# Kernel optimization log

Measured on AMD Instinct MI355X. Metric: run time of the kernel, lower is better.

## Reference

```python
import jax, jax.numpy as jnp
import numpy as np

HEADS = 16
D_MODEL = 1024
GROUP = 4
SEQ = 2048
HEAD_DIM = D_MODEL // HEADS          # 64
KV_HEADS = HEADS // GROUP            # 4


def rope_tables(head_dim, seq_len, base=10000.0):
    # NOTE: faithful to source: exp = -2*arange(0,d,2)/d  (steps of 2 -> base^{-4j/d})
    exp = -2.0 * jnp.arange(0, head_dim, 2, dtype=jnp.float32) / head_dim
    thetas = jnp.power(base, exp)                       # [d/2]
    m = jnp.arange(seq_len, dtype=jnp.float32)          # [S]
    freq = jnp.outer(m, thetas)                         # [S, d/2]
    return jnp.cos(freq), jnp.sin(freq)


def apply_rope(x, cos, sin):
    # x: [B,S,H,D]; complex rotation on consecutive pairs
    B, S, H, D = x.shape
    xr = x.reshape(B, S, H, D // 2, 2)
    x0, x1 = xr[..., 0], xr[..., 1]
    c = cos[None, :S, None, :]
    s = sin[None, :S, None, :]
    out = jnp.stack([x0 * c - x1 * s, x0 * s + x1 * c], axis=-1)
    return out.reshape(B, S, H, D)


def setup_inputs() -> dict:
    key = jax.random.key(0)
    ks = jax.random.split(key, 8)
    B = 1
    q = jax.random.normal(ks[0], (B, SEQ, D_MODEL), dtype=jnp.float32)
    k = jax.random.normal(ks[1], (B, SEQ, D_MODEL), dtype=jnp.float32)
    v = jax.random.normal(ks[2], (B, SEQ, D_MODEL), dtype=jnp.float32)
    mask = jnp.tril(jnp.ones((SEQ, SEQ), dtype=jnp.int32))[None]  # causal [B,S,S]
    sc = 0.02
    Wq = jax.random.normal(ks[3], (D_MODEL, D_MODEL), dtype=jnp.float32) * sc
    Wk = jax.random.normal(ks[4], (D_MODEL, D_MODEL // GROUP), dtype=jnp.float32) * sc
    Wv = jax.random.normal(ks[5], (D_MODEL, D_MODEL // GROUP), dtype=jnp.float32) * sc
    Wo = jax.random.normal(ks[6], (D_MODEL, D_MODEL), dtype=jnp.float32) * sc
    bq = jnp.zeros((D_MODEL,), jnp.float32)
    bk = jnp.zeros((D_MODEL // GROUP,), jnp.float32)
    bv = jnp.zeros((D_MODEL // GROUP,), jnp.float32)
    bo = jnp.zeros((D_MODEL,), jnp.float32)
    return {"q": q, "k": k, "v": v, "mask": mask, "Wq": Wq, "bq": bq,
            "Wk": Wk, "bk": bk, "Wv": Wv, "bv": bv, "Wo": Wo, "bo": bo}


def reference(q, k, v, mask, Wq, bq, Wk, bk, Wv, bv, Wo, bo):
    B, S, _ = q.shape
    cos, sin = rope_tables(HEAD_DIM, S)
    qh = (q @ Wq + bq).reshape(B, S, HEADS, HEAD_DIM)
    kh = (k @ Wk + bk).reshape(B, S, KV_HEADS, HEAD_DIM)
    vh = (v @ Wv + bv).reshape(B, S, KV_HEADS, HEAD_DIM)
    qh = apply_rope(qh, cos, sin)
    kh = apply_rope(kh, cos, sin)
    qh = qh.transpose(0, 2, 1, 3)                       # [B,H,S,D]
    kh = kh.transpose(0, 2, 1, 3)                       # [B,Hkv,S,D]
    vh = vh.transpose(0, 2, 1, 3)
    # torch .repeat tiles: query head j attends kv head j % KV_HEADS
    kh = jnp.tile(kh, (1, GROUP, 1, 1))                 # [B,H,S,D]
    vh = jnp.tile(vh, (1, GROUP, 1, 1))
    scores = jnp.einsum('bhqd,bhkd->bhqk', qh, kh) / jnp.sqrt(
        jnp.asarray(HEAD_DIM, dtype=qh.dtype))
    scores = jnp.where(mask[:, None, :, :] == 0, -jnp.inf, scores)
    attn = jax.nn.softmax(scores, axis=-1)
    out = jnp.einsum('bhqk,bhkd->bhqd', attn, vh)
    out = out.transpose(0, 2, 1, 3).reshape(B, S, D_MODEL)
    return out @ Wo + bo
```

## Files before the change

kernel.cpp:

```cpp
#include <hip/hip_runtime.h>
#include <hip/hip_bf16.h>
#include <math.h>


#define SEQ 2048
#define DM 1024
#define HD 64

using u16 = unsigned short;
typedef __attribute__((ext_vector_type(8))) short bf16x8;
typedef __attribute__((ext_vector_type(4))) float f32x4;

#define QSCALE 0.18033688011112042f

__device__ __forceinline__ u16 f2b(float f) {
    union { float f; unsigned int i; } v; v.f = f;
    unsigned int u = v.i;
    return (u16)((u + 0x7fffu + ((u >> 16) & 1u)) >> 16);
}
__device__ __forceinline__ short f2b_fast(float f) {
    union { float f; unsigned int i; } v; v.f = f;
    return (short)((v.i + 0x8000u) >> 16);
}

__global__ __launch_bounds__(256) void prep_kernel(
    const float* __restrict__ Wq, const float* __restrict__ Wk,
    const float* __restrict__ Wv, const float* __restrict__ Wo,
    u16* __restrict__ Wt, u16* __restrict__ wot)
{
    __shared__ short T[64][72];
    const int tid = blockIdx.x;
    const float* W; u16* dstB; int N, t0, rowoff;
    if (tid < 256)      { W = Wq; dstB = Wt;  N = 1024; t0 = tid;       rowoff = 0; }
    else if (tid < 320) { W = Wk; dstB = Wt;  N = 256;  t0 = tid - 256; rowoff = 1024; }
    else if (tid < 384) { W = Wv; dstB = Wt;  N = 256;  t0 = tid - 320; rowoff = 1280; }
    else                { W = Wo; dstB = wot; N = 1024; t0 = tid - 384; rowoff = 0; }
    const int ntn = N >> 6;
    const int k0 = (t0 / ntn) * 64, n0 = (t0 % ntn) * 64;
    const int t = threadIdx.x;
    {
        const int r = t >> 4, c4 = (t & 15) * 4;
        #pragma unroll
        for (int rr = 0; rr < 4; ++rr) {
            const int k = r + rr * 16;
            float4 wv4 = *reinterpret_cast<const float4*>(W + (size_t)(k0 + k) * N + n0 + c4);
            T[c4 + 0][k] = (short)f2b(wv4.x);
            T[c4 + 1][k] = (short)f2b(wv4.y);
            T[c4 + 2][k] = (short)f2b(wv4.z);
            T[c4 + 3][k] = (short)f2b(wv4.w);
        }
    }
    __syncthreads();
    {
        const int n = t >> 2, ck = (t & 3) * 16;
        u16* dst = dstB + (size_t)(rowoff + n0 + n) * DM + k0 + ck;
        *reinterpret_cast<bf16x8*>(dst)     = *reinterpret_cast<const bf16x8*>(&T[n][ck]);
        *reinterpret_cast<bf16x8*>(dst + 8) = *reinterpret_cast<const bf16x8*>(&T[n][ck + 8]);
    }
}

__global__ __launch_bounds__(256) void proj_mfma(
    const float* __restrict__ qin, const float* __restrict__ kin, const float* __restrict__ vin,
    const u16* __restrict__ Wt,
    const float* __restrict__ bq, const float* __restrict__ bk, const float* __restrict__ bv,
    u16* __restrict__ Qr, u16* __restrict__ Kr, u16* __restrict__ Vrt)
{
    const int n0 = blockIdx.x * 64, m0 = blockIdx.y * 64;
    const int zone = (n0 < 1024) ? 0 : (n0 < 1280) ? 1 : 2;
    const float* __restrict__ src = (zone == 0) ? qin : (zone == 1) ? kin : vin;

    __shared__ short As[64][72];
    __shared__ short Bs[64][72];

    const int t = threadIdx.x;
    const int w = t >> 6, lane = t & 63, lm = lane & 15, quad = lane >> 4;
    const int sr = t >> 2, sc = (t & 3) * 16;

    f32x4 acc[4] = { {0,0,0,0}, {0,0,0,0}, {0,0,0,0}, {0,0,0,0} };

    for (int k0 = 0; k0 < DM; k0 += 64) {
        const float* ap = src + (size_t)(m0 + sr) * DM + k0 + sc;
        float4 a0 = *reinterpret_cast<const float4*>(ap);
        float4 a1 = *reinterpret_cast<const float4*>(ap + 4);
        float4 a2 = *reinterpret_cast<const float4*>(ap + 8);
        float4 a3 = *reinterpret_cast<const float4*>(ap + 12);
        bf16x8 v0, v1;
        v0[0] = (short)f2b(a0.x); v0[1] = (short)f2b(a0.y);
        v0[2] = (short)f2b(a0.z); v0[3] = (short)f2b(a0.w);
        v0[4] = (short)f2b(a1.x); v0[5] = (short)f2b(a1.y);
        v0[6] = (short)f2b(a1.z); v0[7] = (short)f2b(a1.w);
        v1[0] = (short)f2b(a2.x); v1[1] = (short)f2b(a2.y);
        v1[2] = (short)f2b(a2.z); v1[3] = (short)f2b(a2.w);
        v1[4] = (short)f2b(a3.x); v1[5] = (short)f2b(a3.y);
        v1[6] = (short)f2b(a3.z); v1[7] = (short)f2b(a3.w);
        *reinterpret_cast<bf16x8*>(&As[sr][sc])     = v0;
        *reinterpret_cast<bf16x8*>(&As[sr][sc + 8]) = v1;
        const u16* bp = Wt + (size_t)(n0 + sr) * DM + k0 + sc;
        *reinterpret_cast<bf16x8*>(&Bs[sr][sc])     = *reinterpret_cast<const bf16x8*>(bp);
        *reinterpret_cast<bf16x8*>(&Bs[sr][sc + 8]) = *reinterpret_cast<const bf16x8*>(bp + 8);
        __syncthreads();
        bf16x8 af0 = *reinterpret_cast<const bf16x8*>(&As[16 * w + lm][quad * 8]);
        bf16x8 af1 = *reinterpret_cast<const bf16x8*>(&As[16 * w + lm][32 + quad * 8]);
        #pragma unroll
        for (int nb = 0; nb < 4; ++nb) {
            bf16x8 b0 = *reinterpret_cast<const bf16x8*>(&Bs[16 * nb + lm][quad * 8]);
            bf16x8 b1 = *reinterpret_cast<const bf16x8*>(&Bs[16 * nb + lm][32 + quad * 8]);
            acc[nb] = __builtin_amdgcn_mfma_f32_16x16x32_bf16(af0, b0, acc[nb], 0, 0, 0);
            acc[nb] = __builtin_amdgcn_mfma_f32_16x16x32_bf16(af1, b1, acc[nb], 0, 0, 0);
        }
        __syncthreads();
    }

    const float* __restrict__ bias = (zone == 0) ? bq : (zone == 1) ? bk : bv;
    const int nbase = (zone == 0) ? n0 : (zone == 1) ? (n0 - 1024) : (n0 - 1280);
    const int head = nbase >> 6;
    #pragma unroll
    for (int nb = 0; nb < 4; ++nb) {
        const int d = 16 * nb + lm;
        const float bvv = bias[nbase + d];
        float vals[4];
        #pragma unroll
        for (int r = 0; r < 4; ++r) vals[r] = acc[nb][r] + bvv;
        if (zone != 2) {
            const int pi = d >> 1;
            const float theta = exp2f(-0.8304820237f * (float)pi);
            const bool odd = (lm & 1);
            const float sca = (zone == 0) ? QSCALE : 1.0f;
            #pragma unroll
            for (int r = 0; r < 4; ++r) {
                const int m = m0 + 16 * w + quad * 4 + r;
                float sn, cs;
                sincosf((float)m * theta, &sn, &cs);
                float x  = vals[r];
                float xp = __shfl_xor(x, 1);
                vals[r] = (odd ? (xp * sn + x * cs) : (x * cs - xp * sn)) * sca;
            }
        }
        if (zone == 2) {
            u16 pk[4];
            pk[0] = f2b(vals[0]); pk[1] = f2b(vals[1]);
            pk[2] = f2b(vals[2]); pk[3] = f2b(vals[3]);
            u16* vp = Vrt + ((size_t)head * HD + d) * SEQ + m0 + 16 * w + quad * 4;
            *reinterpret_cast<uint2*>(vp) = *reinterpret_cast<uint2*>(pk);
        } else {
            u16* op = (zone == 0 ? Qr : Kr) + (size_t)head * SEQ * HD;
            #pragma unroll
            for (int r = 0; r < 4; ++r) {
                const int m = m0 + 16 * w + quad * 4 + r;
                op[(size_t)m * HD + d] = f2b(vals[r]);
            }
        }
    }
}

__global__ __launch_bounds__(256) void attn_mfma(
    const u16* __restrict__ Qr, const u16* __restrict__ Kr, const u16* __restrict__ Vrt,
    u16* __restrict__ AO)
{
    const int h  = blockIdx.x;
    const int qy = blockIdx.y;
    const int qt = (qy < 16) ? (2 * qy) : (63 - 2 * qy);
    const int kvh = h & 3;

    __shared__ short QPs[64][72];
    __shared__ short Ks[2][64][72];
    __shared__ short Vt[2][64][72];

    const int t = threadIdx.x;
    const int w = t >> 6, lane = t & 63, lm = lane & 15, quad = lane >> 4;
    const int sr = t >> 2, sc = (t & 3) * 16;

    {
        const u16* qp = Qr + ((size_t)h * SEQ + qt * 64 + sr) * HD + sc;
        *reinterpret_cast<bf16x8*>(&QPs[sr][sc])     = *reinterpret_cast<const bf16x8*>(qp);
        *reinterpret_cast<bf16x8*>(&QPs[sr][sc + 8]) = *reinterpret_cast<const bf16x8*>(qp + 8);
    }
    const bf16x8 aq0 = *reinterpret_cast<const bf16x8*>(&QPs[16 * w + lm][quad * 8]);
    const bf16x8 aq1 = *reinterpret_cast<const bf16x8*>(&QPs[16 * w + lm][32 + quad * 8]);

    f32x4 O[4] = { {0,0,0,0}, {0,0,0,0}, {0,0,0,0}, {0,0,0,0} };
    float l_i[4] = { 0.f, 0.f, 0.f, 0.f };

    const u16* kbase = Kr  + ((size_t)kvh * SEQ + sr) * HD + sc;
    const u16* vbase = Vrt + ((size_t)kvh * HD  + sr) * SEQ + sc;
    bf16x8 kA0 = *reinterpret_cast<const bf16x8*>(kbase);
    bf16x8 kA1 = *reinterpret_cast<const bf16x8*>(kbase + 8);
    bf16x8 vA0 = *reinterpret_cast<const bf16x8*>(vbase);
    bf16x8 vA1 = *reinterpret_cast<const bf16x8*>(vbase + 8);

    for (int kt = 0; kt <= qt; ++kt) {
        const int buf = kt & 1;
        *reinterpret_cast<bf16x8*>(&Ks[buf][sr][sc])     = kA0;
        *reinterpret_cast<bf16x8*>(&Ks[buf][sr][sc + 8]) = kA1;
        *reinterpret_cast<bf16x8*>(&Vt[buf][sr][sc])     = vA0;
        *reinterpret_cast<bf16x8*>(&Vt[buf][sr][sc + 8]) = vA1;
        if (kt < qt) {
            const u16* kp = kbase + (size_t)(kt + 1) * 64 * HD;
            const u16* vp = vbase + (size_t)(kt + 1) * 64;
            kA0 = *reinterpret_cast<const bf16x8*>(kp);
            kA1 = *reinterpret_cast<const bf16x8*>(kp + 8);
            vA0 = *reinterpret_cast<const bf16x8*>(vp);
            vA1 = *reinterpret_cast<const bf16x8*>(vp + 8);
        }
        __syncthreads();

        f32x4 s[4];
        #pragma unroll
        for (int nb = 0; nb < 4; ++nb) {
            bf16x8 b0 = *reinterpret_cast<const bf16x8*>(&Ks[buf][16 * nb + lm][quad * 8]);
            bf16x8 b1 = *reinterpret_cast<const bf16x8*>(&Ks[buf][16 * nb + lm][32 + quad * 8]);
            f32x4 zz = { 0.f, 0.f, 0.f, 0.f };
            zz = __builtin_amdgcn_mfma_f32_16x16x32_bf16(aq0, b0, zz, 0, 0, 0);
            s[nb] = __builtin_amdgcn_mfma_f32_16x16x32_bf16(aq1, b1, zz, 0, 0, 0);
        }

        if (kt == qt) {
            #pragma unroll
            for (int nb = 0; nb < 4; ++nb)
                #pragma unroll
                for (int r = 0; r < 4; ++r)
                    if (16 * nb + lm > 16 * w + quad * 4 + r) s[nb][r] = -INFINITY;
        }

        #pragma unroll
        for (int nb = 0; nb < 4; ++nb)
            #pragma unroll
            for (int r = 0; r < 4; ++r) {
                float e = __builtin_amdgcn_exp2f(fminf(s[nb][r], 126.f));
                l_i[r] += e;
                QPs[16 * w + quad * 4 + r][16 * nb + lm] = f2b_fast(e);
            }

        bf16x8 ap0 = *reinterpret_cast<const bf16x8*>(&QPs[16 * w + lm][quad * 8]);
        bf16x8 ap1 = *reinterpret_cast<const bf16x8*>(&QPs[16 * w + lm][32 + quad * 8]);
        #pragma unroll
        for (int db = 0; db < 4; ++db) {
            bf16x8 b0 = *reinterpret_cast<const bf16x8*>(&Vt[buf][16 * db + lm][quad * 8]);
            bf16x8 b1 = *reinterpret_cast<const bf16x8*>(&Vt[buf][16 * db + lm][32 + quad * 8]);
            O[db] = __builtin_amdgcn_mfma_f32_16x16x32_bf16(ap0, b0, O[db], 0, 0, 0);
            O[db] = __builtin_amdgcn_mfma_f32_16x16x32_bf16(ap1, b1, O[db], 0, 0, 0);
        }
    }

    #pragma unroll
    for (int r = 0; r < 4; ++r) {
        float lr = l_i[r];
        #pragma unroll
        for (int off = 1; off < 16; off <<= 1)
            lr += __shfl_xor(lr, off);
        const float inv = 1.0f / lr;
        const size_t row = (size_t)(qt * 64 + 16 * w + quad * 4 + r) * DM + (size_t)h * HD;
        #pragma unroll
        for (int db = 0; db < 4; ++db)
            AO[row + 16 * db + lm] = f2b(O[db][r] * inv);
    }
}

__global__ __launch_bounds__(256) void oproj_mfma(
    const u16* __restrict__ AO, const u16* __restrict__ wot,
    const float* __restrict__ bo, float* __restrict__ out)
{
    __shared__ short As[64][72];
    __shared__ short Bs[64][72];
    const int t = threadIdx.x;
    const int w = t >> 6, lane = t & 63, lm = lane & 15, quad = lane >> 4;
    const int m0 = blockIdx.y * 64, n0 = blockIdx.x * 64;
    const int sr = t >> 2, sc = (t & 3) * 16;

    f32x4 acc[4] = { {0,0,0,0}, {0,0,0,0}, {0,0,0,0}, {0,0,0,0} };

    for (int k0 = 0; k0 < DM; k0 += 64) {
        const u16* ap = AO + (size_t)(m0 + sr) * DM + k0 + sc;
        *reinterpret_cast<bf16x8*>(&As[sr][sc])     = *reinterpret_cast<const bf16x8*>(ap);
        *reinterpret_cast<bf16x8*>(&As[sr][sc + 8]) = *reinterpret_cast<const bf16x8*>(ap + 8);
        const u16* bp = wot + (size_t)(n0 + sr) * DM + k0 + sc;
        *reinterpret_cast<bf16x8*>(&Bs[sr][sc])     = *reinterpret_cast<const bf16x8*>(bp);
        *reinterpret_cast<bf16x8*>(&Bs[sr][sc + 8]) = *reinterpret_cast<const bf16x8*>(bp + 8);
        __syncthreads();
        bf16x8 af0 = *reinterpret_cast<const bf16x8*>(&As[16 * w + lm][quad * 8]);
        bf16x8 af1 = *reinterpret_cast<const bf16x8*>(&As[16 * w + lm][32 + quad * 8]);
        #pragma unroll
        for (int nb = 0; nb < 4; ++nb) {
            bf16x8 b0 = *reinterpret_cast<const bf16x8*>(&Bs[16 * nb + lm][quad * 8]);
            bf16x8 b1 = *reinterpret_cast<const bf16x8*>(&Bs[16 * nb + lm][32 + quad * 8]);
            acc[nb] = __builtin_amdgcn_mfma_f32_16x16x32_bf16(af0, b0, acc[nb], 0, 0, 0);
            acc[nb] = __builtin_amdgcn_mfma_f32_16x16x32_bf16(af1, b1, acc[nb], 0, 0, 0);
        }
        __syncthreads();
    }

    #pragma unroll
    for (int nb = 0; nb < 4; ++nb) {
        const int dl = 16 * nb + lm;
        const float bv = bo[n0 + dl];
        #pragma unroll
        for (int r = 0; r < 4; ++r) {
            const int m = m0 + 16 * w + quad * 4 + r;
            out[(size_t)m * DM + n0 + dl] = acc[nb][r] + bv;
        }
    }
}

extern "C" void kernel_launch(void* const* d_in, const int* in_sizes, int n_in,
                              void* d_out, int out_size, void* d_ws, size_t ws_size,
                              hipStream_t stream)
{
    const float* q  = (const float*)d_in[0];
    const float* k  = (const float*)d_in[1];
    const float* v  = (const float*)d_in[2];
    const float* Wq = (const float*)d_in[4];
    const float* bq = (const float*)d_in[5];
    const float* Wk = (const float*)d_in[6];
    const float* bk = (const float*)d_in[7];
    const float* Wv = (const float*)d_in[8];
    const float* bv = (const float*)d_in[9];
    const float* Wo = (const float*)d_in[10];
    const float* bo = (const float*)d_in[11];
    float* out = (float*)d_out;

    u16* Wt  = (u16*)d_ws;
    u16* wot = Wt  + (size_t)1536 * 1024;
    u16* Qr  = wot + (size_t)1024 * 1024;
    u16* Kr  = Qr  + (size_t)16 * SEQ * HD;
    u16* Vrt = Kr  + (size_t)4 * SEQ * HD;
    u16* AO  = Vrt + (size_t)4 * SEQ * HD;

    hipLaunchKernelGGL(prep_kernel, dim3(640), dim3(256), 0, stream,
                       Wq, Wk, Wv, Wo, Wt, wot);
    hipLaunchKernelGGL(proj_mfma, dim3(24, 32), dim3(256), 0, stream,
                       q, k, v, Wt, bq, bk, bv, Qr, Kr, Vrt);
    hipLaunchKernelGGL(attn_mfma, dim3(16, 32), dim3(256), 0, stream,
                       Qr, Kr, Vrt, AO);
    hipLaunchKernelGGL(oproj_mfma, dim3(16, 32), dim3(256), 0, stream,
                       AO, wot, bo, out);
}
```

Before: 174.8 us.

## Pre-tile bf16 operands and use 128x128 double-buffered direct-to-LDS GEMMs

The prep kernel now also converts the q/k/v activations to bf16 and writes them, along with the weights, in a k-chunked tiled layout. Attention writes its output in the same tiled layout. The projection and output GEMMs move from 64x64 tiles to 128x128 tiles with a 4x4 MFMA block per wave, and they stream operands through global_load_lds into double-buffered LDS. This is meant to raise data reuse per tile and overlap loads with compute, at the cost of an extra activation conversion pass, more workspace, fewer blocks per GEMM and higher register use.

```diff
diff --git a/kernel.cpp b/kernel.cpp
--- a/kernel.cpp
+++ b/kernel.cpp
@@ -23,131 +23,180 @@
     return (short)((v.i + 0x8000u) >> 16);
 }
 
+__device__ __forceinline__ void gl2lds16(const u16* g, u16* l) {
+    __builtin_amdgcn_global_load_lds(
+        (const __attribute__((address_space(1))) unsigned int*)g,
+        (__attribute__((address_space(3))) unsigned int*)l, 16, 0, 0);
+}
+
 __global__ __launch_bounds__(256) void prep_kernel(
+    const float* __restrict__ qin, const float* __restrict__ kin, const float* __restrict__ vin,
     const float* __restrict__ Wq, const float* __restrict__ Wk,
     const float* __restrict__ Wv, const float* __restrict__ Wo,
+    u16* __restrict__ Xq, u16* __restrict__ Xk, u16* __restrict__ Xv,
     u16* __restrict__ Wt, u16* __restrict__ wot)
 {
     __shared__ short T[64][72];
-    const int tid = blockIdx.x;
-    const float* W; u16* dstB; int N, t0, rowoff;
-    if (tid < 256)      { W = Wq; dstB = Wt;  N = 1024; t0 = tid;       rowoff = 0; }
-    else if (tid < 320) { W = Wk; dstB = Wt;  N = 256;  t0 = tid - 256; rowoff = 1024; }
-    else if (tid < 384) { W = Wv; dstB = Wt;  N = 256;  t0 = tid - 320; rowoff = 1280; }
-    else                { W = Wo; dstB = wot; N = 1024; t0 = tid - 384; rowoff = 0; }
-    const int ntn = N >> 6;
-    const int k0 = (t0 / ntn) * 64, n0 = (t0 % ntn) * 64;
+    const int b = blockIdx.x;
     const int t = threadIdx.x;
-    {
+
+    if (b < 640) {
+        const float* W; u16* dst; int N, t0, rowoff;
+        if (b < 256)      { W = Wq; dst = Wt;  N = 1024; t0 = b;       rowoff = 0; }
+        else if (b < 320) { W = Wk; dst = Wt;  N = 256;  t0 = b - 256; rowoff = 1024; }
+        else if (b < 384) { W = Wv; dst = Wt;  N = 256;  t0 = b - 320; rowoff = 1280; }
+        else              { W = Wo; dst = wot; N = 1024; t0 = b - 384; rowoff = 0; }
+        const int ntn = N >> 6;
+        const int k0 = (t0 / ntn) * 64, n0 = (t0 % ntn) * 64;
         const int r = t >> 4, c4 = (t & 15) * 4;
         #pragma unroll
         for (int rr = 0; rr < 4; ++rr) {
             const int k = r + rr * 16;
-            float4 wv4 = *reinterpret_cast<const float4*>(W + (size_t)(k0 + k) * N + n0 + c4);
-            T[c4 + 0][k] = (short)f2b(wv4.x);
-            T[c4 + 1][k] = (short)f2b(wv4.y);
-            T[c4 + 2][k] = (short)f2b(wv4.z);
-            T[c4 + 3][k] = (short)f2b(wv4.w);
-        }
-    }
-    __syncthreads();
-    {
-        const int n = t >> 2, ck = (t & 3) * 16;
-        u16* dst = dstB + (size_t)(rowoff + n0 + n) * DM + k0 + ck;
-        *reinterpret_cast<bf16x8*>(dst)     = *reinterpret_cast<const bf16x8*>(&T[n][ck]);
-        *reinterpret_cast<bf16x8*>(dst + 8) = *reinterpret_cast<const bf16x8*>(&T[n][ck + 8]);
+            float4 w4 = *reinterpret_cast<const float4*>(W + (size_t)(k0 + k) * N + n0 + c4);
+            T[c4 + 0][k] = (short)f2b(w4.x);
+            T[c4 + 1][k] = (short)f2b(w4.y);
+            T[c4 + 2][k] = (short)f2b(w4.z);
+            T[c4 + 3][k] = (short)f2b(w4.w);
+        }
+        __syncthreads();
+        const int tk = k0 >> 6;
+        #pragma unroll
+        for (int p = 0; p < 2; ++p) {
+            const int c = t + p * 256;
+            const int n = c & 63, kc = c >> 6;
+            const int ng = rowoff + n0 + n;
+            const int nt = ng >> 7, nr = ng & 127;
+            u16* dp = dst + ((size_t)((nt * 16 + tk) * 8 + kc)) * 1024 + nr * 8;
+            *reinterpret_cast<bf16x8*>(dp) = *reinterpret_cast<const bf16x8*>(&T[n][kc * 8]);
+        }
+    } else {
+        const int idx = b - 640;
+        const int which = idx >> 9;
+        const int ib = idx & 511;
+        const int m0 = (ib >> 4) * 64, tk = ib & 15, k0 = tk * 64;
+        const float* src = (which == 0) ? qin : (which == 1) ? kin : vin;
+        u16* dst = (which == 0) ? Xq : (which == 1) ? Xk : Xv;
+        const int m = t >> 4, kq = (t & 15) * 4;
+        #pragma unroll
+        for (int mm = 0; mm < 4; ++mm) {
+            const int ml = mm * 16 + m;
+            float4 x4 = *reinterpret_cast<const float4*>(src + (size_t)(m0 + ml) * DM + k0 + kq);
+            T[ml][kq + 0] = (short)f2b(x4.x);
+            T[ml][kq + 1] = (short)f2b(x4.y);
+            T[ml][kq + 2] = (short)f2b(x4.z);
+            T[ml][kq + 3] = (short)f2b(x4.w);
+        }
+        __syncthreads();
+        #pragma unroll
+        for (int p = 0; p < 2; ++p) {
+            const int c = t + p * 256;
+            const int ml = c & 63, kc = c >> 6;
+            const int mg = m0 + ml;
+            const int tr = mg >> 7, mr = mg & 127;
+            u16* dp = dst + ((size_t)((tr * 16 + tk) * 8 + kc)) * 1024 + mr * 8;
+            *reinterpret_cast<bf16x8*>(dp) = *reinterpret_cast<const bf16x8*>(&T[ml][kc * 8]);
+        }
     }
 }
 
 __global__ __launch_bounds__(256) void proj_mfma(
-    const float* __restrict__ qin, const float* __restrict__ kin, const float* __restrict__ vin,
+    const u16* __restrict__ Xq, const u16* __restrict__ Xk, const u16* __restrict__ Xv,
     const u16* __restrict__ Wt,
     const float* __restrict__ bq, const float* __restrict__ bk, const float* __restrict__ bv,
     u16* __restrict__ Qr, u16* __restrict__ Kr, u16* __restrict__ Vrt)
 {
-    const int n0 = blockIdx.x * 64, m0 = blockIdx.y * 64;
-    const int zone = (n0 < 1024) ? 0 : (n0 < 1280) ? 1 : 2;
-    const float* __restrict__ src = (zone == 0) ? qin : (zone == 1) ? kin : vin;
-
-    __shared__ short As[64][72];
-    __shared__ short Bs[64][72];
+    const int nt = blockIdx.x, mt = blockIdx.y;
+    const int zone = (nt < 8) ? 0 : (nt < 10) ? 1 : 2;
+    const u16* __restrict__ Az = (zone == 0) ? Xq : (zone == 1) ? Xk : Xv;
+
+    __shared__ u16 As[2][8192];
+    __shared__ u16 Bs[2][8192];
 
     const int t = threadIdx.x;
     const int w = t >> 6, lane = t & 63, lm = lane & 15, quad = lane >> 4;
-    const int sr = t >> 2, sc = (t & 3) * 16;
-
-    f32x4 acc[4] = { {0,0,0,0}, {0,0,0,0}, {0,0,0,0}, {0,0,0,0} };
-
-    for (int k0 = 0; k0 < DM; k0 += 64) {
-        const float* ap = src + (size_t)(m0 + sr) * DM + k0 + sc;
-        float4 a0 = *reinterpret_cast<const float4*>(ap);
-        float4 a1 = *reinterpret_cast<const float4*>(ap + 4);
-        float4 a2 = *reinterpret_cast<const float4*>(ap + 8);
-        float4 a3 = *reinterpret_cast<const float4*>(ap + 12);
-        bf16x8 v0, v1;
-        v0[0] = (short)f2b(a0.x); v0[1] = (short)f2b(a0.y);
-        v0[2] = (short)f2b(a0.z); v0[3] = (short)f2b(a0.w);
-        v0[4] = (short)f2b(a1.x); v0[5] = (short)f2b(a1.y);
-        v0[6] = (short)f2b(a1.z); v0[7] = (short)f2b(a1.w);
-        v1[0] = (short)f2b(a2.x); v1[1] = (short)f2b(a2.y);
-        v1[2] = (short)f2b(a2.z); v1[3] = (short)f2b(a2.w);
-        v1[4] = (short)f2b(a3.x); v1[5] = (short)f2b(a3.y);
-        v1[6] = (short)f2b(a3.z); v1[7] = (short)f2b(a3.w);
-        *reinterpret_cast<bf16x8*>(&As[sr][sc])     = v0;
-        *reinterpret_cast<bf16x8*>(&As[sr][sc + 8]) = v1;
-        const u16* bp = Wt + (size_t)(n0 + sr) * DM + k0 + sc;
-        *reinterpret_cast<bf16x8*>(&Bs[sr][sc])     = *reinterpret_cast<const bf16x8*>(bp);
-        *reinterpret_cast<bf16x8*>(&Bs[sr][sc + 8]) = *reinterpret_cast<const bf16x8*>(bp + 8);
+    const int wy = w >> 1, wx = w & 1;
+
+    f32x4 acc[4][4];
+    #pragma unroll
+    for (int i = 0; i < 4; ++i)
+        #pragma unroll
+        for (int j = 0; j < 4; ++j) acc[i][j] = (f32x4){0.f, 0.f, 0.f, 0.f};
+
+    {
+        const u16* ga = Az + ((size_t)(mt * 16 + 0) << 13);
+        const u16* gb = Wt + ((size_t)(nt * 16 + 0) << 13);
+        #pragma unroll
+        for (int g = 0; g < 4; ++g) {
+            gl2lds16(ga + (size_t)(g * 256 + t) * 8, &As[0][(g * 256 + w * 64) * 8]);
+            gl2lds16(gb + (size_t)(g * 256 + t) * 8, &Bs[0][(g * 256 + w * 64) * 8]);
+        }
+    }
+
+    for (int tk = 0; tk < 16; ++tk) {
+        const int buf = tk & 1;
         __syncthreads();
-        bf16x8 af0 = *reinterpret_cast<const bf16x8*>(&As[16 * w + lm][quad * 8]);
-        bf16x8 af1 = *reinterpret_cast<const bf16x8*>(&As[16 * w + lm][32 + quad * 8]);
-        #pragma unroll
-        for (int nb = 0; nb < 4; ++nb) {
-            bf16x8 b0 = *reinterpret_cast<const bf16x8*>(&Bs[16 * nb + lm][quad * 8]);
-            bf16x8 b1 = *reinterpret_cast<const bf16x8*>(&Bs[16 * nb + lm][32 + quad * 8]);
-            acc[nb] = __builtin_amdgcn_mfma_f32_16x16x32_bf16(af0, b0, acc[nb], 0, 0, 0);
-            acc[nb] = __builtin_amdgcn_mfma_f32_16x16x32_bf16(af1, b1, acc[nb], 0, 0, 0);
-        }
-        __syncthreads();
+        if (tk < 15) {
+            const u16* ga = Az + ((size_t)(mt * 16 + tk + 1) << 13);
+            const u16* gb = Wt + ((size_t)(nt * 16 + tk + 1) << 13);
+            #pragma unroll
+            for (int g = 0; g < 4; ++g) {
+                gl2lds16(ga + (size_t)(g * 256 + t) * 8, &As[buf ^ 1][(g * 256 + w * 64) * 8]);
+                gl2lds16(gb + (size_t)(g * 256 + t) * 8, &Bs[buf ^ 1][(g * 256 + w * 64) * 8]);
+            }
+        }
+        #pragma unroll
+        for (int w2 = 0; w2 < 2; ++w2) {
+            const int kc = w2 * 4 + quad;
+            bf16x8 af[4], bfv[4];
+            #pragma unroll
+            for (int mb = 0; mb < 4; ++mb)
+                af[mb] = *reinterpret_cast<const bf16x8*>(&As[buf][kc * 1024 + (wy * 64 + mb * 16 + lm) * 8]);
+            #pragma unroll
+            for (int nb = 0; nb < 4; ++nb)
+                bfv[nb] = *reinterpret_cast<const bf16x8*>(&Bs[buf][kc * 1024 + (wx * 64 + nb * 16 + lm) * 8]);
+            #pragma unroll
+            for (int mb = 0; mb < 4; ++mb)
+                #pragma unroll
+                for (int nb = 0; nb < 4; ++nb)
+                    acc[mb][nb] = __builtin_amdgcn_mfma_f32_16x16x32_bf16(af[mb], bfv[nb], acc[mb][nb], 0, 0, 0);
+        }
     }
 
     const float* __restrict__ bias = (zone == 0) ? bq : (zone == 1) ? bk : bv;
-    const int nbase = (zone == 0) ? n0 : (zone == 1) ? (n0 - 1024) : (n0 - 1280);
-    const int head = nbase >> 6;
+    const int zoff = (zone == 0) ? 0 : (zone == 1) ? 1024 : 1280;
     #pragma unroll
     for (int nb = 0; nb < 4; ++nb) {
-        const int d = 16 * nb + lm;
-        const float bvv = bias[nbase + d];
-        float vals[4];
-        #pragma unroll
-        for (int r = 0; r < 4; ++r) vals[r] = acc[nb][r] + bvv;
+        const int ncol = nt * 128 + wx * 64 + nb * 16 + lm;
+        const int nl = ncol - zoff;
+        const int h = nl >> 6, d = nl & 63;
+        const float bvv = bias[nl];
         if (zone != 2) {
             const int pi = d >> 1;
             const float theta = exp2f(-0.8304820237f * (float)pi);
-            const bool odd = (lm & 1);
+            const bool odd = (d & 1);
             const float sca = (zone == 0) ? QSCALE : 1.0f;
-            #pragma unroll
-            for (int r = 0; r < 4; ++r) {
-                const int m = m0 + 16 * w + quad * 4 + r;
-                float sn, cs;
-                sincosf((float)m * theta, &sn, &cs);
-                float x  = vals[r];
-                float xp = __shfl_xor(x, 1);
-                vals[r] = (odd ? (xp * sn + x * cs) : (x * cs - xp * sn)) * sca;
-            }
-        }
-        if (zone == 2) {
-            u16 pk[4];
-            pk[0] = f2b(vals[0]); pk[1] = f2b(vals[1]);
-            pk[2] = f2b(vals[2]); pk[3] = f2b(vals[3]);
-            u16* vp = Vrt + ((size_t)head * HD + d) * SEQ + m0 + 16 * w + quad * 4;
-            *reinterpret_cast<uint2*>(vp) = *reinterpret_cast<uint2*>(pk);
+            u16* op = (zone == 0 ? Qr : Kr) + (size_t)h * SEQ * HD;
+            #pragma unroll
+            for (int mb = 0; mb < 4; ++mb)
+                #pragma unroll
+                for (int r = 0; r < 4; ++r) {
+                    const int m = mt * 128 + wy * 64 + mb * 16 + quad * 4 + r;
+                    float x = acc[mb][nb][r] + bvv;
+                    float sn, cs;
+                    sincosf((float)m * theta, &sn, &cs);
+                    float xp = __shfl_xor(x, 1);
+                    float o = (odd ? (xp * sn + x * cs) : (x * cs - xp * sn)) * sca;
+                    op[(size_t)m * HD + d] = f2b(o);
+                }
         } else {
-            u16* op = (zone == 0 ? Qr : Kr) + (size_t)head * SEQ * HD;
-            #pragma unroll
-            for (int r = 0; r < 4; ++r) {
-                const int m = m0 + 16 * w + quad * 4 + r;
-                op[(size_t)m * HD + d] = f2b(vals[r]);
+            #pragma unroll
+            for (int mb = 0; mb < 4; ++mb) {
+                const int m = mt * 128 + wy * 64 + mb * 16 + quad * 4;
+                u16 pk[4];
+                #pragma unroll
+                for (int r = 0; r < 4; ++r) pk[r] = f2b(acc[mb][nb][r] + bvv);
+                u16* vp = Vrt + ((size_t)h * HD + d) * SEQ + m;
+                *reinterpret_cast<uint2*>(vp) = *reinterpret_cast<uint2*>(pk);
             }
         }
     }
@@ -249,10 +298,14 @@
         for (int off = 1; off < 16; off <<= 1)
             lr += __shfl_xor(lr, off);
         const float inv = 1.0f / lr;
-        const size_t row = (size_t)(qt * 64 + 16 * w + quad * 4 + r) * DM + (size_t)h * HD;
-        #pragma unroll
-        for (int db = 0; db < 4; ++db)
-            AO[row + 16 * db + lm] = f2b(O[db][r] * inv);
+        const int row = qt * 64 + 16 * w + quad * 4 + r;
+        const int tr = row >> 7, mr = row & 127;
+        const int j = lm & 7;
+        #pragma unroll
+        for (int db = 0; db < 4; ++db) {
+            const int kc = 2 * db + (lm >> 3);
+            AO[((size_t)((tr * 16 + h) * 8 + kc)) * 1024 + mr * 8 + j] = f2b(O[db][r] * inv);
+        }
     }
 }
 
@@ -260,44 +313,72 @@
     const u16* __restrict__ AO, const u16* __restrict__ wot,
     const float* __restrict__ bo, float* __restrict__ out)
 {
-    __shared__ short As[64][72];
-    __shared__ short Bs[64][72];
+    const int nt = blockIdx.x, mt = blockIdx.y;
+
+    __shared__ u16 As[2][8192];
+    __shared__ u16 Bs[2][8192];
+
     const int t = threadIdx.x;
     const int w = t >> 6, lane = t & 63, lm = lane & 15, quad = lane >> 4;
-    const int m0 = blockIdx.y * 64, n0 = blockIdx.x * 64;
-    const int sr = t >> 2, sc = (t & 3) * 16;
-
-    f32x4 acc[4] = { {0,0,0,0}, {0,0,0,0}, {0,0,0,0}, {0,0,0,0} };
-
-    for (int k0 = 0; k0 < DM; k0 += 64) {
-        const u16* ap = AO + (size_t)(m0 + sr) * DM + k0 + sc;
-        *reinterpret_cast<bf16x8*>(&As[sr][sc])     = *reinterpret_cast<const bf16x8*>(ap);
-        *reinterpret_cast<bf16x8*>(&As[sr][sc + 8]) = *reinterpret_cast<const bf16x8*>(ap + 8);
-        const u16* bp = wot + (size_t)(n0 + sr) * DM + k0 + sc;
-        *reinterpret_cast<bf16x8*>(&Bs[sr][sc])     = *reinterpret_cast<const bf16x8*>(bp);
-        *reinterpret_cast<bf16x8*>(&Bs[sr][sc + 8]) = *reinterpret_cast<const bf16x8*>(bp + 8);
+    const int wy = w >> 1, wx = w & 1;
+
+    f32x4 acc[4][4];
+    #pragma unroll
+    for (int i = 0; i < 4; ++i)
+        #pragma unroll
+        for (int j = 0; j < 4; ++j) acc[i][j] = (f32x4){0.f, 0.f, 0.f, 0.f};
+
+    {
+        const u16* ga = AO  + ((size_t)(mt * 16 + 0) << 13);
+        const u16* gb = wot + ((size_t)(nt * 16 + 0) << 13);
+        #pragma unroll
+        for (int g = 0; g < 4; ++g) {
+            gl2lds16(ga + (size_t)(g * 256 + t) * 8, &As[0][(g * 256 + w * 64) * 8]);
+            gl2lds16(gb + (size_t)(g * 256 + t) * 8, &Bs[0][(g * 256 + w * 64) * 8]);
+        }
+    }
+
+    for (int tk = 0; tk < 16; ++tk) {
+        const int buf = tk & 1;
         __syncthreads();
-        bf16x8 af0 = *reinterpret_cast<const bf16x8*>(&As[16 * w + lm][quad * 8]);
-        bf16x8 af1 = *reinterpret_cast<const bf16x8*>(&As[16 * w + lm][32 + quad * 8]);
-        #pragma unroll
-        for (int nb = 0; nb < 4; ++nb) {
-            bf16x8 b0 = *reinterpret_cast<const bf16x8*>(&Bs[16 * nb + lm][quad * 8]);
-            bf16x8 b1 = *reinterpret_cast<const bf16x8*>(&Bs[16 * nb + lm][32 + quad * 8]);
-            acc[nb] = __builtin_amdgcn_mfma_f32_16x16x32_bf16(af0, b0, acc[nb], 0, 0, 0);
-            acc[nb] = __builtin_amdgcn_mfma_f32_16x16x32_bf16(af1, b1, acc[nb], 0, 0, 0);
-        }
-        __syncthreads();
+        if (tk < 15) {
+            const u16* ga = AO  + ((size_t)(mt * 16 + tk + 1) << 13);
+            const u16* gb = wot + ((size_t)(nt * 16 + tk + 1) << 13);
+            #pragma unroll
+            for (int g = 0; g < 4; ++g) {
+                gl2lds16(ga + (size_t)(g * 256 + t) * 8, &As[buf ^ 1][(g * 256 + w * 64) * 8]);
+                gl2lds16(gb + (size_t)(g * 256 + t) * 8, &Bs[buf ^ 1][(g * 256 + w * 64) * 8]);
+            }
+        }
+        #pragma unroll
+        for (int w2 = 0; w2 < 2; ++w2) {
+            const int kc = w2 * 4 + quad;
+            bf16x8 af[4], bfv[4];
+            #pragma unroll
+            for (int mb = 0; mb < 4; ++mb)
+                af[mb] = *reinterpret_cast<const bf16x8*>(&As[buf][kc * 1024 + (wy * 64 + mb * 16 + lm) * 8]);
+            #pragma unroll
+            for (int nb = 0; nb < 4; ++nb)
+                bfv[nb] = *reinterpret_cast<const bf16x8*>(&Bs[buf][kc * 1024 + (wx * 64 + nb * 16 + lm) * 8]);
+            #pragma unroll
+            for (int mb = 0; mb < 4; ++mb)
+                #pragma unroll
+                for (int nb = 0; nb < 4; ++nb)
+                    acc[mb][nb] = __builtin_amdgcn_mfma_f32_16x16x32_bf16(af[mb], bfv[nb], acc[mb][nb], 0, 0, 0);
+        }
     }
 
     #pragma unroll
     for (int nb = 0; nb < 4; ++nb) {
-        const int dl = 16 * nb + lm;
-        const float bv = bo[n0 + dl];
-        #pragma unroll
-        for (int r = 0; r < 4; ++r) {
-            const int m = m0 + 16 * w + quad * 4 + r;
-            out[(size_t)m * DM + n0 + dl] = acc[nb][r] + bv;
-        }
+        const int ncol = nt * 128 + wx * 64 + nb * 16 + lm;
+        const float bvv = bo[ncol];
+        #pragma unroll
+        for (int mb = 0; mb < 4; ++mb)
+            #pragma unroll
+            for (int r = 0; r < 4; ++r) {
+                const int m = mt * 128 + wy * 64 + mb * 16 + quad * 4 + r;
+                out[(size_t)m * DM + ncol] = acc[mb][nb][r] + bvv;
+            }
     }
 }
 
@@ -318,19 +399,22 @@
     const float* bo = (const float*)d_in[11];
     float* out = (float*)d_out;
 
-    u16* Wt  = (u16*)d_ws;
+    u16* Xq  = (u16*)d_ws;
+    u16* Xk  = Xq  + (size_t)SEQ * DM;
+    u16* Xv  = Xk  + (size_t)SEQ * DM;
+    u16* Wt  = Xv  + (size_t)SEQ * DM;
     u16* wot = Wt  + (size_t)1536 * 1024;
     u16* Qr  = wot + (size_t)1024 * 1024;
     u16* Kr  = Qr  + (size_t)16 * SEQ * HD;
     u16* Vrt = Kr  + (size_t)4 * SEQ * HD;
     u16* AO  = Vrt + (size_t)4 * SEQ * HD;
 
-    hipLaunchKernelGGL(prep_kernel, dim3(640), dim3(256), 0, stream,
-                       Wq, Wk, Wv, Wo, Wt, wot);
-    hipLaunchKernelGGL(proj_mfma, dim3(24, 32), dim3(256), 0, stream,
-                       q, k, v, Wt, bq, bk, bv, Qr, Kr, Vrt);
+    hipLaunchKernelGGL(prep_kernel, dim3(2176), dim3(256), 0, stream,
+                       q, k, v, Wq, Wk, Wv, Wo, Xq, Xk, Xv, Wt, wot);
+    hipLaunchKernelGGL(proj_mfma, dim3(12, 16), dim3(256), 0, stream,
+                       Xq, Xk, Xv, Wt, bq, bk, bv, Qr, Kr, Vrt);
     hipLaunchKernelGGL(attn_mfma, dim3(16, 32), dim3(256), 0, stream,
                        Qr, Kr, Vrt, AO);
-    hipLaunchKernelGGL(oproj_mfma, dim3(16, 32), dim3(256), 0, stream,
+    hipLaunchKernelGGL(oproj_mfma, dim3(8, 16), dim3(256), 0, stream,
                        AO, wot, bo, out);
 }
```

After: 222.5 us. +27.3%, slower.

## Pre-convert activations to bf16 and restructure attention to split keys across waves

Applied to the files above, without the earlier changes.

The prep kernel now also converts the q/k/v fp32 activations to bf16 once, so each projection block stops re-reading fp32 rows and reconverting them for every N tile. The attention kernel is reorganized: each wave owns a slice of keys for all 64 queries and processes two key tiles per iteration with a transposed score computation. Partial outputs are reduced across waves through shared memory at the end. This trades extra workspace traffic, more LDS and registers, and a serialized cross-wave reduction for fewer redundant conversions and larger PV MFMA chunks per sync.

```diff
diff --git a/kernel.cpp b/kernel.cpp
--- a/kernel.cpp
+++ b/kernel.cpp
@@ -18,56 +18,75 @@
     unsigned int u = v.i;
     return (u16)((u + 0x7fffu + ((u >> 16) & 1u)) >> 16);
 }
-__device__ __forceinline__ short f2b_fast(float f) {
+__device__ __forceinline__ u16 f2b_fast(float f) {
     union { float f; unsigned int i; } v; v.f = f;
-    return (short)((v.i + 0x8000u) >> 16);
+    return (u16)((v.i + 0x8000u) >> 16);
 }
 
 __global__ __launch_bounds__(256) void prep_kernel(
+    const float* __restrict__ qin, const float* __restrict__ kin, const float* __restrict__ vin,
     const float* __restrict__ Wq, const float* __restrict__ Wk,
     const float* __restrict__ Wv, const float* __restrict__ Wo,
+    u16* __restrict__ Xq, u16* __restrict__ Xk, u16* __restrict__ Xv,
     u16* __restrict__ Wt, u16* __restrict__ wot)
 {
-    __shared__ short T[64][72];
-    const int tid = blockIdx.x;
-    const float* W; u16* dstB; int N, t0, rowoff;
-    if (tid < 256)      { W = Wq; dstB = Wt;  N = 1024; t0 = tid;       rowoff = 0; }
-    else if (tid < 320) { W = Wk; dstB = Wt;  N = 256;  t0 = tid - 256; rowoff = 1024; }
-    else if (tid < 384) { W = Wv; dstB = Wt;  N = 256;  t0 = tid - 320; rowoff = 1280; }
-    else                { W = Wo; dstB = wot; N = 1024; t0 = tid - 384; rowoff = 0; }
-    const int ntn = N >> 6;
-    const int k0 = (t0 / ntn) * 64, n0 = (t0 % ntn) * 64;
+    const int b = blockIdx.x;
     const int t = threadIdx.x;
-    {
+
+    if (b < 640) {
+        __shared__ short T[64][72];
+        const float* W; u16* dst; int N, t0, rowoff;
+        if (b < 256)      { W = Wq; dst = Wt;  N = 1024; t0 = b;       rowoff = 0; }
+        else if (b < 320) { W = Wk; dst = Wt;  N = 256;  t0 = b - 256; rowoff = 1024; }
+        else if (b < 384) { W = Wv; dst = Wt;  N = 256;  t0 = b - 320; rowoff = 1280; }
+        else              { W = Wo; dst = wot; N = 1024; t0 = b - 384; rowoff = 0; }
+        const int ntn = N >> 6;
+        const int k0 = (t0 / ntn) * 64, n0 = (t0 % ntn) * 64;
         const int r = t >> 4, c4 = (t & 15) * 4;
         #pragma unroll
         for (int rr = 0; rr < 4; ++rr) {
             const int k = r + rr * 16;
-            float4 wv4 = *reinterpret_cast<const float4*>(W + (size_t)(k0 + k) * N + n0 + c4);
-            T[c4 + 0][k] = (short)f2b(wv4.x);
-            T[c4 + 1][k] = (short)f2b(wv4.y);
-            T[c4 + 2][k] = (short)f2b(wv4.z);
-            T[c4 + 3][k] = (short)f2b(wv4.w);
-        }
-    }
-    __syncthreads();
-    {
+            float4 w4 = *reinterpret_cast<const float4*>(W + (size_t)(k0 + k) * N + n0 + c4);
+            T[c4 + 0][k] = (short)f2b(w4.x);
+            T[c4 + 1][k] = (short)f2b(w4.y);
+            T[c4 + 2][k] = (short)f2b(w4.z);
+            T[c4 + 3][k] = (short)f2b(w4.w);
+        }
+        __syncthreads();
         const int n = t >> 2, ck = (t & 3) * 16;
-        u16* dst = dstB + (size_t)(rowoff + n0 + n) * DM + k0 + ck;
-        *reinterpret_cast<bf16x8*>(dst)     = *reinterpret_cast<const bf16x8*>(&T[n][ck]);
-        *reinterpret_cast<bf16x8*>(dst + 8) = *reinterpret_cast<const bf16x8*>(&T[n][ck + 8]);
+        u16* dp = dst + (size_t)(rowoff + n0 + n) * DM + k0 + ck;
+        *reinterpret_cast<bf16x8*>(dp)     = *reinterpret_cast<const bf16x8*>(&T[n][ck]);
+        *reinterpret_cast<bf16x8*>(dp + 8) = *reinterpret_cast<const bf16x8*>(&T[n][ck + 8]);
+    } else {
+        const int idx = b - 640;
+        const int which = idx >> 8;
+        const int ib = idx & 255;
+        const float* src = (which == 0) ? qin : (which == 1) ? kin : vin;
+        u16* dst = (which == 0) ? Xq : (which == 1) ? Xk : Xv;
+        const size_t base = (size_t)ib * 8192 + (size_t)t * 32;
+        #pragma unroll
+        for (int c = 0; c < 4; ++c) {
+            float4 x0 = *reinterpret_cast<const float4*>(src + base + c * 8);
+            float4 x1 = *reinterpret_cast<const float4*>(src + base + c * 8 + 4);
+            bf16x8 o;
+            o[0] = (short)f2b(x0.x); o[1] = (short)f2b(x0.y);
+            o[2] = (short)f2b(x0.z); o[3] = (short)f2b(x0.w);
+            o[4] = (short)f2b(x1.x); o[5] = (short)f2b(x1.y);
+            o[6] = (short)f2b(x1.z); o[7] = (short)f2b(x1.w);
+            *reinterpret_cast<bf16x8*>(dst + base + c * 8) = o;
+        }
     }
 }
 
 __global__ __launch_bounds__(256) void proj_mfma(
-    const float* __restrict__ qin, const float* __restrict__ kin, const float* __restrict__ vin,
+    const u16* __restrict__ Xq, const u16* __restrict__ Xk, const u16* __restrict__ Xv,
     const u16* __restrict__ Wt,
     const float* __restrict__ bq, const float* __restrict__ bk, const float* __restrict__ bv,
     u16* __restrict__ Qr, u16* __restrict__ Kr, u16* __restrict__ Vrt)
 {
     const int n0 = blockIdx.x * 64, m0 = blockIdx.y * 64;
     const int zone = (n0 < 1024) ? 0 : (n0 < 1280) ? 1 : 2;
-    const float* __restrict__ src = (zone == 0) ? qin : (zone == 1) ? kin : vin;
+    const u16* __restrict__ Az = (zone == 0) ? Xq : (zone == 1) ? Xk : Xv;
 
     __shared__ short As[64][72];
     __shared__ short Bs[64][72];
@@ -79,22 +98,9 @@
     f32x4 acc[4] = { {0,0,0,0}, {0,0,0,0}, {0,0,0,0}, {0,0,0,0} };
 
     for (int k0 = 0; k0 < DM; k0 += 64) {
-        const float* ap = src + (size_t)(m0 + sr) * DM + k0 + sc;
-        float4 a0 = *reinterpret_cast<const float4*>(ap);
-        float4 a1 = *reinterpret_cast<const float4*>(ap + 4);
-        float4 a2 = *reinterpret_cast<const float4*>(ap + 8);
-        float4 a3 = *reinterpret_cast<const float4*>(ap + 12);
-        bf16x8 v0, v1;
-        v0[0] = (short)f2b(a0.x); v0[1] = (short)f2b(a0.y);
-        v0[2] = (short)f2b(a0.z); v0[3] = (short)f2b(a0.w);
-        v0[4] = (short)f2b(a1.x); v0[5] = (short)f2b(a1.y);
-        v0[6] = (short)f2b(a1.z); v0[7] = (short)f2b(a1.w);
-        v1[0] = (short)f2b(a2.x); v1[1] = (short)f2b(a2.y);
-        v1[2] = (short)f2b(a2.z); v1[3] = (short)f2b(a2.w);
-        v1[4] = (short)f2b(a3.x); v1[5] = (short)f2b(a3.y);
-        v1[6] = (short)f2b(a3.z); v1[7] = (short)f2b(a3.w);
-        *reinterpret_cast<bf16x8*>(&As[sr][sc])     = v0;
-        *reinterpret_cast<bf16x8*>(&As[sr][sc + 8]) = v1;
+        const u16* ap = Az + (size_t)(m0 + sr) * DM + k0 + sc;
+        *reinterpret_cast<bf16x8*>(&As[sr][sc])     = *reinterpret_cast<const bf16x8*>(ap);
+        *reinterpret_cast<bf16x8*>(&As[sr][sc + 8]) = *reinterpret_cast<const bf16x8*>(ap + 8);
         const u16* bp = Wt + (size_t)(n0 + sr) * DM + k0 + sc;
         *reinterpret_cast<bf16x8*>(&Bs[sr][sc])     = *reinterpret_cast<const bf16x8*>(bp);
         *reinterpret_cast<bf16x8*>(&Bs[sr][sc + 8]) = *reinterpret_cast<const bf16x8*>(bp + 8);
@@ -135,20 +141,18 @@
                 float xp = __shfl_xor(x, 1);
                 vals[r] = (odd ? (xp * sn + x * cs) : (x * cs - xp * sn)) * sca;
             }
-        }
-        if (zone == 2) {
-            u16 pk[4];
-            pk[0] = f2b(vals[0]); pk[1] = f2b(vals[1]);
-            pk[2] = f2b(vals[2]); pk[3] = f2b(vals[3]);
-            u16* vp = Vrt + ((size_t)head * HD + d) * SEQ + m0 + 16 * w + quad * 4;
-            *reinterpret_cast<uint2*>(vp) = *reinterpret_cast<uint2*>(pk);
-        } else {
             u16* op = (zone == 0 ? Qr : Kr) + (size_t)head * SEQ * HD;
             #pragma unroll
             for (int r = 0; r < 4; ++r) {
                 const int m = m0 + 16 * w + quad * 4 + r;
                 op[(size_t)m * HD + d] = f2b(vals[r]);
             }
+        } else {
+            u16 pk[4];
+            #pragma unroll
+            for (int r = 0; r < 4; ++r) pk[r] = f2b(vals[r]);
+            u16* vp = Vrt + ((size_t)head * HD + d) * SEQ + m0 + 16 * w + quad * 4;
+            *reinterpret_cast<uint2*>(vp) = *reinterpret_cast<uint2*>(pk);
         }
     }
 }
@@ -162,97 +166,148 @@
     const int qt = (qy < 16) ? (2 * qy) : (63 - 2 * qy);
     const int kvh = h & 3;
 
-    __shared__ short QPs[64][72];
+    __shared__ short Qs[64][72];
     __shared__ short Ks[2][64][72];
-    __shared__ short Vt[2][64][72];
+    __shared__ short Vt[64][136];
+    __shared__ short Ps[64][136];
+    __shared__ float Lred[4][64];
 
     const int t = threadIdx.x;
     const int w = t >> 6, lane = t & 63, lm = lane & 15, quad = lane >> 4;
     const int sr = t >> 2, sc = (t & 3) * 16;
+    const int colb = (sc >> 4) * 32;
 
     {
         const u16* qp = Qr + ((size_t)h * SEQ + qt * 64 + sr) * HD + sc;
-        *reinterpret_cast<bf16x8*>(&QPs[sr][sc])     = *reinterpret_cast<const bf16x8*>(qp);
-        *reinterpret_cast<bf16x8*>(&QPs[sr][sc + 8]) = *reinterpret_cast<const bf16x8*>(qp + 8);
-    }
-    const bf16x8 aq0 = *reinterpret_cast<const bf16x8*>(&QPs[16 * w + lm][quad * 8]);
-    const bf16x8 aq1 = *reinterpret_cast<const bf16x8*>(&QPs[16 * w + lm][32 + quad * 8]);
-
-    f32x4 O[4] = { {0,0,0,0}, {0,0,0,0}, {0,0,0,0}, {0,0,0,0} };
-    float l_i[4] = { 0.f, 0.f, 0.f, 0.f };
-
+        *reinterpret_cast<bf16x8*>(&Qs[sr][sc])     = *reinterpret_cast<const bf16x8*>(qp);
+        *reinterpret_cast<bf16x8*>(&Qs[sr][sc + 8]) = *reinterpret_cast<const bf16x8*>(qp + 8);
+    }
+    __syncthreads();
+    bf16x8 bq[4][2];
+    #pragma unroll
+    for (int nb = 0; nb < 4; ++nb) {
+        bq[nb][0] = *reinterpret_cast<const bf16x8*>(&Qs[16 * nb + lm][quad * 8]);
+        bq[nb][1] = *reinterpret_cast<const bf16x8*>(&Qs[16 * nb + lm][32 + quad * 8]);
+    }
+
+    f32x4 O[4][4];
+    #pragma unroll
+    for (int i = 0; i < 4; ++i)
+        #pragma unroll
+        for (int j = 0; j < 4; ++j) O[i][j] = (f32x4){0.f, 0.f, 0.f, 0.f};
+    float lp[4] = { 0.f, 0.f, 0.f, 0.f };
+
+    const int ntile = qt + 1;
     const u16* kbase = Kr  + ((size_t)kvh * SEQ + sr) * HD + sc;
     const u16* vbase = Vrt + ((size_t)kvh * HD  + sr) * SEQ + sc;
-    bf16x8 kA0 = *reinterpret_cast<const bf16x8*>(kbase);
-    bf16x8 kA1 = *reinterpret_cast<const bf16x8*>(kbase + 8);
-    bf16x8 vA0 = *reinterpret_cast<const bf16x8*>(vbase);
-    bf16x8 vA1 = *reinterpret_cast<const bf16x8*>(vbase + 8);
-
-    for (int kt = 0; kt <= qt; ++kt) {
-        const int buf = kt & 1;
-        *reinterpret_cast<bf16x8*>(&Ks[buf][sr][sc])     = kA0;
-        *reinterpret_cast<bf16x8*>(&Ks[buf][sr][sc + 8]) = kA1;
-        *reinterpret_cast<bf16x8*>(&Vt[buf][sr][sc])     = vA0;
-        *reinterpret_cast<bf16x8*>(&Vt[buf][sr][sc + 8]) = vA1;
-        if (kt < qt) {
-            const u16* kp = kbase + (size_t)(kt + 1) * 64 * HD;
-            const u16* vp = vbase + (size_t)(kt + 1) * 64;
-            kA0 = *reinterpret_cast<const bf16x8*>(kp);
-            kA1 = *reinterpret_cast<const bf16x8*>(kp + 8);
-            vA0 = *reinterpret_cast<const bf16x8*>(vp);
-            vA1 = *reinterpret_cast<const bf16x8*>(vp + 8);
-        }
-        __syncthreads();
-
-        f32x4 s[4];
-        #pragma unroll
-        for (int nb = 0; nb < 4; ++nb) {
-            bf16x8 b0 = *reinterpret_cast<const bf16x8*>(&Ks[buf][16 * nb + lm][quad * 8]);
-            bf16x8 b1 = *reinterpret_cast<const bf16x8*>(&Ks[buf][16 * nb + lm][32 + quad * 8]);
-            f32x4 zz = { 0.f, 0.f, 0.f, 0.f };
-            zz = __builtin_amdgcn_mfma_f32_16x16x32_bf16(aq0, b0, zz, 0, 0, 0);
-            s[nb] = __builtin_amdgcn_mfma_f32_16x16x32_bf16(aq1, b1, zz, 0, 0, 0);
-        }
-
-        if (kt == qt) {
-            #pragma unroll
-            for (int nb = 0; nb < 4; ++nb)
+
+    for (int u = 0; u < ntile; u += 2) {
+        const bool has1 = (u + 1 < ntile);
+        {
+            const u16* kp0 = kbase + (size_t)u * 64 * HD;
+            *reinterpret_cast<bf16x8*>(&Ks[0][sr][sc])     = *reinterpret_cast<const bf16x8*>(kp0);
+            *reinterpret_cast<bf16x8*>(&Ks[0][sr][sc + 8]) = *reinterpret_cast<const bf16x8*>(kp0 + 8);
+            const u16* vp0 = vbase + (size_t)u * 64;
+            *reinterpret_cast<bf16x8*>(&Vt[sr][colb])      = *reinterpret_cast<const bf16x8*>(vp0);
+            *reinterpret_cast<bf16x8*>(&Vt[sr][colb + 8])  = *reinterpret_cast<const bf16x8*>(vp0 + 8);
+            if (has1) {
+                const u16* kp1 = kbase + (size_t)(u + 1) * 64 * HD;
+                *reinterpret_cast<bf16x8*>(&Ks[1][sr][sc])     = *reinterpret_cast<const bf16x8*>(kp1);
+                *reinterpret_cast<bf16x8*>(&Ks[1][sr][sc + 8]) = *reinterpret_cast<const bf16x8*>(kp1 + 8);
+                const u16* vp1 = vbase + (size_t)(u + 1) * 64;
+                *reinterpret_cast<bf16x8*>(&Vt[sr][colb + 16]) = *reinterpret_cast<const bf16x8*>(vp1);
+                *reinterpret_cast<bf16x8*>(&Vt[sr][colb + 24]) = *reinterpret_cast<const bf16x8*>(vp1 + 8);
+            } else {
+                bf16x8 z = {0,0,0,0,0,0,0,0};
+                *reinterpret_cast<bf16x8*>(&Vt[sr][colb + 16]) = z;
+                *reinterpret_cast<bf16x8*>(&Vt[sr][colb + 24]) = z;
+            }
+        }
+        __syncthreads();
+
+        #pragma unroll
+        for (int tp = 0; tp < 2; ++tp) {
+            const int kt = u + tp;
+            if (tp == 1 && !has1) {
+                const uint2 z2 = make_uint2(0u, 0u);
                 #pragma unroll
-                for (int r = 0; r < 4; ++r)
-                    if (16 * nb + lm > 16 * w + quad * 4 + r) s[nb][r] = -INFINITY;
-        }
-
-        #pragma unroll
-        for (int nb = 0; nb < 4; ++nb)
-            #pragma unroll
-            for (int r = 0; r < 4; ++r) {
-                float e = __builtin_amdgcn_exp2f(fminf(s[nb][r], 126.f));
-                l_i[r] += e;
-                QPs[16 * w + quad * 4 + r][16 * nb + lm] = f2b_fast(e);
-            }
-
-        bf16x8 ap0 = *reinterpret_cast<const bf16x8*>(&QPs[16 * w + lm][quad * 8]);
-        bf16x8 ap1 = *reinterpret_cast<const bf16x8*>(&QPs[16 * w + lm][32 + quad * 8]);
+                for (int nb = 0; nb < 4; ++nb)
+                    *reinterpret_cast<uint2*>(&Ps[16 * nb + lm][w * 32 + 16 + quad * 4]) = z2;
+                continue;
+            }
+            const bf16x8 ak0 = *reinterpret_cast<const bf16x8*>(&Ks[tp][16 * w + lm][quad * 8]);
+            const bf16x8 ak1 = *reinterpret_cast<const bf16x8*>(&Ks[tp][16 * w + lm][32 + quad * 8]);
+            const bool diag = (kt == qt);
+            #pragma unroll
+            for (int nb = 0; nb < 4; ++nb) {
+                f32x4 ss = { 0.f, 0.f, 0.f, 0.f };
+                ss = __builtin_amdgcn_mfma_f32_16x16x32_bf16(ak0, bq[nb][0], ss, 0, 0, 0);
+                ss = __builtin_amdgcn_mfma_f32_16x16x32_bf16(ak1, bq[nb][1], ss, 0, 0, 0);
+                u16 pk[4];
+                #pragma unroll
+                for (int r = 0; r < 4; ++r) {
+                    float sv = ss[r];
+                    if (diag && (16 * w + quad * 4 + r > 16 * nb + lm)) sv = -INFINITY;
+                    float e = __builtin_amdgcn_exp2f(fminf(sv, 126.f));
+                    lp[nb] += e;
+                    pk[r] = f2b_fast(e);
+                }
+                *reinterpret_cast<uint2*>(&Ps[16 * nb + lm][w * 32 + tp * 16 + quad * 4]) =
+                    *reinterpret_cast<uint2*>(pk);
+            }
+        }
+
         #pragma unroll
         for (int db = 0; db < 4; ++db) {
-            bf16x8 b0 = *reinterpret_cast<const bf16x8*>(&Vt[buf][16 * db + lm][quad * 8]);
-            bf16x8 b1 = *reinterpret_cast<const bf16x8*>(&Vt[buf][16 * db + lm][32 + quad * 8]);
-            O[db] = __builtin_amdgcn_mfma_f32_16x16x32_bf16(ap0, b0, O[db], 0, 0, 0);
-            O[db] = __builtin_amdgcn_mfma_f32_16x16x32_bf16(ap1, b1, O[db], 0, 0, 0);
-        }
-    }
-
-    #pragma unroll
-    for (int r = 0; r < 4; ++r) {
-        float lr = l_i[r];
-        #pragma unroll
-        for (int off = 1; off < 16; off <<= 1)
-            lr += __shfl_xor(lr, off);
-        const float inv = 1.0f / lr;
-        const size_t row = (size_t)(qt * 64 + 16 * w + quad * 4 + r) * DM + (size_t)h * HD;
-        #pragma unroll
-        for (int db = 0; db < 4; ++db)
-            AO[row + 16 * db + lm] = f2b(O[db][r] * inv);
+            const bf16x8 av = *reinterpret_cast<const bf16x8*>(&Vt[16 * db + lm][w * 32 + quad * 8]);
+            #pragma unroll
+            for (int nb = 0; nb < 4; ++nb) {
+                const bf16x8 bp = *reinterpret_cast<const bf16x8*>(&Ps[16 * nb + lm][w * 32 + quad * 8]);
+                O[db][nb] = __builtin_amdgcn_mfma_f32_16x16x32_bf16(av, bp, O[db][nb], 0, 0, 0);
+            }
+        }
+        __syncthreads();
+    }
+
+    #pragma unroll
+    for (int nb = 0; nb < 4; ++nb) {
+        lp[nb] += __shfl_xor(lp[nb], 16);
+        lp[nb] += __shfl_xor(lp[nb], 32);
+    }
+    if (quad == 0) {
+        #pragma unroll
+        for (int nb = 0; nb < 4; ++nb) Lred[w][16 * nb + lm] = lp[nb];
+    }
+
+    float* Sf = reinterpret_cast<float*>(&Ps[0][0]);
+    #pragma unroll
+    for (int ph = 0; ph < 4; ++ph) {
+        __syncthreads();
+        if (w == ph) {
+            #pragma unroll
+            for (int db = 0; db < 4; ++db)
+                #pragma unroll
+                for (int nb = 0; nb < 4; ++nb)
+                    #pragma unroll
+                    for (int r = 0; r < 4; ++r) {
+                        const int d = 16 * db + quad * 4 + r, q = 16 * nb + lm;
+                        const float v = O[db][nb][r];
+                        Sf[q * 68 + d] = (ph == 0) ? v : (Sf[q * 68 + d] + v);
+                    }
+        }
+    }
+    __syncthreads();
+
+    {
+        const int q = t >> 2, dc = (t & 3) * 16;
+        const float linv = 1.0f / (Lred[0][q] + Lred[1][q] + Lred[2][q] + Lred[3][q]);
+        u16 pk[16];
+        #pragma unroll
+        for (int j = 0; j < 16; ++j)
+            pk[j] = f2b(Sf[q * 68 + dc + j] * linv);
+        u16* op = AO + (size_t)(qt * 64 + q) * DM + h * HD + dc;
+        *reinterpret_cast<bf16x8*>(op)     = *reinterpret_cast<const bf16x8*>(pk);
+        *reinterpret_cast<bf16x8*>(op + 8) = *reinterpret_cast<const bf16x8*>(pk + 8);
     }
 }
 
@@ -318,17 +373,20 @@
     const float* bo = (const float*)d_in[11];
     float* out = (float*)d_out;
 
-    u16* Wt  = (u16*)d_ws;
+    u16* Xq  = (u16*)d_ws;
+    u16* Xk  = Xq  + (size_t)SEQ * DM;
+    u16* Xv  = Xk  + (size_t)SEQ * DM;
+    u16* Wt  = Xv  + (size_t)SEQ * DM;
     u16* wot = Wt  + (size_t)1536 * 1024;
     u16* Qr  = wot + (size_t)1024 * 1024;
     u16* Kr  = Qr  + (size_t)16 * SEQ * HD;
     u16* Vrt = Kr  + (size_t)4 * SEQ * HD;
     u16* AO  = Vrt + (size_t)4 * SEQ * HD;
 
-    hipLaunchKernelGGL(prep_kernel, dim3(640), dim3(256), 0, stream,
-                       Wq, Wk, Wv, Wo, Wt, wot);
+    hipLaunchKernelGGL(prep_kernel, dim3(1408), dim3(256), 0, stream,
+                       q, k, v, Wq, Wk, Wv, Wo, Xq, Xk, Xv, Wt, wot);
     hipLaunchKernelGGL(proj_mfma, dim3(24, 32), dim3(256), 0, stream,
-                       q, k, v, Wt, bq, bk, bv, Qr, Kr, Vrt);
+                       Xq, Xk, Xv, Wt, bq, bk, bv, Qr, Kr, Vrt);
     hipLaunchKernelGGL(attn_mfma, dim3(16, 32), dim3(256), 0, stream,
                        Qr, Kr, Vrt, AO);
     hipLaunchKernelGGL(oproj_mfma, dim3(16, 32), dim3(256), 0, stream,
```

New measurement: 184.0 us. 1.05x slower.
